# Optimization experiments

Measured on AMD Instinct MI355X. Metric: run time of the kernel, lower is better.

## Reference

```python
import jax, jax.numpy as jnp
import numpy as np

N_ITEMS = 50000; LM_IN = 768; D = 128; B = 256; L = 50
NH = 2; NL = 2; FF = 4 * D
TEMP = 0.1; BETA1 = 0.5; BETA2 = 0.5
NEG = -1e9


def _ln(x, g, b, eps=1e-5):
    m = x.mean(-1, keepdims=True)
    v = ((x - m) ** 2).mean(-1, keepdims=True)
    return (x - m) / jnp.sqrt(v + eps) * g + b


def _encoder(h, mask, P):
    # SASRec/BERT-style TransformerEncoder: pos-emb + LN, then NL blocks of
    # causal+padding-masked MHA and GELU FFN with post-LN residuals.
    pos, ln0g, ln0b, Wqkv, bqkv, Wo, bo, l1g, l1b, W1, b1, W2, b2, l2g, l2b = P
    Bh, Lh, Dh = h.shape
    dh = Dh // NH
    keep = jnp.tril(jnp.broadcast_to((mask != 0)[:, None, None, :], (Bh, 1, Lh, Lh)))
    bias = jnp.where(keep, 0.0, NEG)  # additive attention mask, [B,1,L,L]
    h = _ln(h + pos, ln0g, ln0b)
    scale = float(1.0 / np.sqrt(dh))
    for l in range(NL):
        qkv = h @ Wqkv[l] + bqkv[l]
        q, k, v = jnp.split(qkv, 3, axis=-1)
        sp = lambda t: t.reshape(Bh, Lh, NH, dh).transpose(0, 2, 1, 3)
        q, k, v = sp(q), sp(k), sp(v)
        att = jax.nn.softmax(jnp.einsum('bhqd,bhkd->bhqk', q, k) * scale + bias, axis=-1)
        o = jnp.einsum('bhqk,bhkd->bhqd', att, v).transpose(0, 2, 1, 3).reshape(Bh, Lh, Dh)
        h = _ln(h + o @ Wo[l] + bo[l], l1g[l], l1b[l])
        f = jax.nn.gelu(h @ W1[l] + b1[l]) @ W2[l] + b2[l]
        h = _ln(h + f, l2g[l], l2b[l])
    return h


def _last(trans, mask):
    # gather embedding at the last valid position: index = mask.sum(1) - 1
    idx = mask.sum(1).astype(jnp.int32) - 1
    return jnp.take_along_axis(trans, idx[:, None, None], axis=1)[:, 0]


def setup_inputs():
    key = jax.random.key(0)
    ks = jax.random.split(key, 32)
    s = 0.02

    def p(i, shape):
        return jax.random.normal(ks[i], shape, jnp.float32) * s

    inp = {}
    inp['x'] = jax.random.normal(ks[0], (N_ITEMS, LM_IN), jnp.float32)
    inp['uid'] = jax.random.randint(ks[1], (B,), 0, 100000)
    inp['edge_index'] = jax.random.randint(ks[2], (2, 1000), 0, N_ITEMS)
    inp['max_itemid'] = N_ITEMS - 1
    inp['itemid'] = jax.random.randint(ks[3], (B, L), 0, N_ITEMS)
    inp['mask'] = jnp.ones((B, L), jnp.float32)
    inp['id_emb'] = p(4, (N_ITEMS, D))
    inp['id_ln_g'] = jnp.ones(D); inp['id_ln_b'] = jnp.zeros(D)
    inp['text_W'] = p(5, (LM_IN, D)); inp['text_b'] = jnp.zeros(D)
    inp['text_ln_g'] = jnp.ones(D); inp['text_ln_b'] = jnp.zeros(D)
    for pre, base in (('ide_', 6), ('te_', 16)):
        inp[pre + 'pos'] = p(base, (L, D))
        inp[pre + 'ln0_g'] = jnp.ones(D); inp[pre + 'ln0_b'] = jnp.zeros(D)
        inp[pre + 'Wqkv'] = p(base + 1, (NL, D, 3 * D)); inp[pre + 'bqkv'] = jnp.zeros((NL, 3 * D))
        inp[pre + 'Wo'] = p(base + 2, (NL, D, D)); inp[pre + 'bo'] = jnp.zeros((NL, D))
        inp[pre + 'ln1_g'] = jnp.ones((NL, D)); inp[pre + 'ln1_b'] = jnp.zeros((NL, D))
        inp[pre + 'W1'] = p(base + 3, (NL, D, FF)); inp[pre + 'b1'] = jnp.zeros((NL, FF))
        inp[pre + 'W2'] = p(base + 4, (NL, FF, D)); inp[pre + 'b2'] = jnp.zeros((NL, D))
        inp[pre + 'ln2_g'] = jnp.ones((NL, D)); inp[pre + 'ln2_b'] = jnp.zeros((NL, D))
    return inp


def reference(x, uid, edge_index, max_itemid, itemid, mask,
              id_emb, id_ln_g, id_ln_b, text_W, text_b, text_ln_g, text_ln_b,
              ide_pos, ide_ln0_g, ide_ln0_b, ide_Wqkv, ide_bqkv, ide_Wo, ide_bo,
              ide_ln1_g, ide_ln1_b, ide_W1, ide_b1, ide_W2, ide_b2, ide_ln2_g, ide_ln2_b,
              te_pos, te_ln0_g, te_ln0_b, te_Wqkv, te_bqkv, te_Wo, te_bo,
              te_ln1_g, te_ln1_b, te_W1, te_b1, te_W2, te_b2, te_ln2_g, te_ln2_b):
    # --- ID module: layernorm over the full embedding table, gather, encode ---
    gnn_emb = _ln(id_emb, id_ln_g, id_ln_b)  # [n_items, D]
    ideP = (ide_pos, ide_ln0_g, ide_ln0_b, ide_Wqkv, ide_bqkv, ide_Wo, ide_bo,
            ide_ln1_g, ide_ln1_b, ide_W1, ide_b1, ide_W2, ide_b2, ide_ln2_g, ide_ln2_b)
    trans = _encoder(gnn_emb[itemid], mask, ideP)  # [B,L,D]
    session_emb = _last(trans, mask)  # [B,D]
    item_embs = gnn_emb[:max_itemid + 1]
    scores1 = session_emb @ item_embs.T  # [B, n_items]
    # --- Text module: linear+relu (dropout off at eval), layernorm, encode ---
    xmap = _ln(jax.nn.relu(x @ text_W + text_b), text_ln_g, text_ln_b)  # [n_items, D]
    teP = (te_pos, te_ln0_g, te_ln0_b, te_Wqkv, te_bqkv, te_Wo, te_bo,
           te_ln1_g, te_ln1_b, te_W1, te_b1, te_W2, te_b2, te_ln2_g, te_ln2_b)
    trans2 = _encoder(xmap[itemid], mask, teP)
    session_feat = _last(trans2, mask)
    scores2 = (session_feat @ xmap[:max_itemid + 1].T) / TEMP
    # eval path: combined score
    scores = BETA1 * scores1 + BETA2 * scores2
    return (scores, scores1, scores2, item_embs, gnn_emb[:max_itemid + 1], xmap[:max_itemid + 1])
```

## Files before the change

kernel.cpp:

```cpp
#include <hip/hip_runtime.h>

#define DEV __device__ __forceinline__

typedef float f32x4 __attribute__((ext_vector_type(4)));
typedef __bf16 bf16x8 __attribute__((ext_vector_type(8)));
#define MFMA16(a,b,c) __builtin_amdgcn_mfma_f32_16x16x32_bf16(a,b,c,0,0,0)

#define ASTRIDE 136
#define QSTRIDE 72
#define PSTRIDE 132

DEV float wsum(float v){
  #pragma unroll
  for (int o = 32; o > 0; o >>= 1) v += __shfl_xor(v, o, 64);
  return v;
}

DEV float gelu_f(float x){
  float u = 0.7978845608028654f * (x + 0.044715f * x * x * x);
  float e = __expf(2.f * u);
  float th = 1.f - 2.f / (e + 1.f);
  return 0.5f * x * (1.f + th);
}

__global__ __launch_bounds__(256) void ln_kernel(const float* in,
    float* out0, float* out1,
    const float* __restrict__ g, const float* __restrict__ bb, int nrows)
{
  int w = threadIdx.x >> 6, l = threadIdx.x & 63;
  int row = blockIdx.x * 4 + w;
  if (row >= nrows) return;
  const float* rp = in + (size_t)row * 128;
  float v0 = rp[l], v1 = rp[l + 64];
  float m = wsum(v0 + v1) * 0.0078125f;
  float d0 = v0 - m, d1 = v1 - m;
  float var = wsum(d0 * d0 + d1 * d1) * 0.0078125f;
  float rs = rsqrtf(var + 1e-5f);
  float o0 = d0 * rs * g[l] + bb[l];
  float o1 = d1 * rs * g[l + 64] + bb[l + 64];
  size_t base = (size_t)row * 128;
  out0[base + l] = o0; out0[base + l + 64] = o1;
  if (out1){ out1[base + l] = o0; out1[base + l + 64] = o1; }
}

__global__ __launch_bounds__(256) void prep_w(
    const float* __restrict__ Wa, const float* __restrict__ Wb,
    __bf16* __restrict__ dst, int K, int N, int nmat)
{
  int tid = blockIdx.x * 256 + threadIdx.x;
  int tpm = (N >> 4) * (K >> 5);
  if (tid >= nmat * tpm * 64) return;
  int lane = tid & 63;
  int tile = (tid >> 6) % tpm;
  int mat  = tid / (tpm * 64);
  const float* W;
  if (nmat == 1) W = Wa;
  else W = ((mat >> 1) ? Wb : Wa) + (size_t)(mat & 1) * K * N;
  int kdiv = K >> 5;
  int nt = tile / kdiv, kt = tile - nt * kdiv;
  int col  = nt * 16 + (lane & 15);
  int krow = kt * 32 + (lane >> 4) * 8;
  __bf16 v[8];
  #pragma unroll
  for (int j = 0; j < 8; j++) v[j] = (__bf16)W[(size_t)(krow + j) * N + col];
  *(bf16x8*)(dst + (size_t)tid * 8) = *(bf16x8*)v;
}

__global__ __launch_bounds__(256) void xmap_mfma(
    const float* __restrict__ X, const __bf16* __restrict__ wt,
    const float* __restrict__ bias, float* __restrict__ out)
{
  __shared__ __bf16 xb[64 * ASTRIDE];
  const int t = threadIdx.x, w = t >> 6, l = t & 63, lm = l & 15, quad = l >> 4;
  const int r0 = blockIdx.x * 64;
  f32x4 acc[8];
  #pragma unroll
  for (int nt = 0; nt < 8; nt++) acc[nt] = (f32x4){0.f,0.f,0.f,0.f};
  for (int kc = 0; kc < 6; kc++){
    for (int i = t; i < 64 * 32; i += 256){
      int r = i >> 5, c4 = (i & 31) * 4;
      float4 v = make_float4(0.f,0.f,0.f,0.f);
      if (r0 + r < 50000) v = *(const float4*)&X[(size_t)(r0 + r) * 768 + kc * 128 + c4];
      xb[r*ASTRIDE + c4 + 0] = (__bf16)v.x;
      xb[r*ASTRIDE + c4 + 1] = (__bf16)v.y;
      xb[r*ASTRIDE + c4 + 2] = (__bf16)v.z;
      xb[r*ASTRIDE + c4 + 3] = (__bf16)v.w;
    }
    __syncthreads();
    bf16x8 af[4];
    #pragma unroll
    for (int kt = 0; kt < 4; kt++)
      af[kt] = *(const bf16x8*)&xb[(w*16 + lm)*ASTRIDE + kt*32 + quad*8];
    #pragma unroll
    for (int nt = 0; nt < 8; nt++)
      #pragma unroll
      for (int kt = 0; kt < 4; kt++)
        acc[nt] = MFMA16(af[kt], *(const bf16x8*)(wt + ((size_t)(nt*24 + kc*4 + kt)*64 + l)*8), acc[nt]);
    __syncthreads();
  }
  #pragma unroll
  for (int nt = 0; nt < 8; nt++){
    int n = nt*16 + lm;
    float bs = bias[n];
    #pragma unroll
    for (int r = 0; r < 4; r++){
      int row = r0 + w*16 + quad*4 + r;
      if (row < 50000) out[(size_t)row*128 + n] = fmaxf(acc[nt][r] + bs, 0.f);
    }
  }
}

struct EncP {
  const float *pos, *ln0g, *ln0b, *bqkv, *bo, *ln1g, *ln1b, *b1, *b2, *ln2g, *ln2b;
  const __bf16 *wq, *wo, *w1, *w2;
  const float* emb;
  float* outT;
};

DEV void ln_reg(float res[8][4], const float* g, const float* bb, int lm){
  float gv[8], bv[8];
  #pragma unroll
  for (int nt = 0; nt < 8; nt++){ gv[nt] = g[nt*16 + lm]; bv[nt] = bb[nt*16 + lm]; }
  #pragma unroll
  for (int r = 0; r < 4; r++){
    float s = 0.f;
    #pragma unroll
    for (int nt = 0; nt < 8; nt++) s += res[nt][r];
    s += __shfl_xor(s, 1, 64); s += __shfl_xor(s, 2, 64);
    s += __shfl_xor(s, 4, 64); s += __shfl_xor(s, 8, 64);
    float mean = s * 0.0078125f;
    float v = 0.f;
    #pragma unroll
    for (int nt = 0; nt < 8; nt++){ float d = res[nt][r] - mean; v += d * d; }
    v += __shfl_xor(v, 1, 64); v += __shfl_xor(v, 2, 64);
    v += __shfl_xor(v, 4, 64); v += __shfl_xor(v, 8, 64);
    float rs = rsqrtf(v * 0.0078125f + 1e-5f);
    #pragma unroll
    for (int nt = 0; nt < 8; nt++)
      res[nt][r] = (res[nt][r] - mean) * rs * gv[nt] + bv[nt];
  }
}

DEV void stage_res(const float res[8][4], __bf16* ab, int mb, int quad, int lm){
  #pragma unroll
  for (int r = 0; r < 4; r++){
    int m = mb + quad*4 + r;
    #pragma unroll
    for (int nt = 0; nt < 8; nt++)
      ab[m*ASTRIDE + nt*16 + lm] = (__bf16)res[nt][r];
  }
}

__global__ __launch_bounds__(256, 4) void encoder_mfma(
    EncP P0, EncP P1, const int* __restrict__ itemid, const float* __restrict__ mask)
{
  EncP P = (blockIdx.x < 256) ? P0 : P1;
  const int b = blockIdx.x & 255;
  const int t = threadIdx.x, w = t >> 6, l = t & 63;
  const int lm = l & 15, quad = l >> 4;
  const int mb = w * 16;
  const int am = mb + lm;

  __shared__ __align__(16) char pool[35840];
  __bf16* ab = (__bf16*)pool;
  __bf16* kb = (__bf16*)(pool + 17408);
  __bf16* vb = (__bf16*)(pool + 17408 + 9216);
  float*  hfp = (float*)pool;
  __shared__ float maskv[64];

  if (t < 64) maskv[t] = (t < 50) ? mask[b*50 + t] : 0.f;

  for (int r = w; r < 50; r += 4){
    int it = itemid[b*50 + r];
    const float* er = P.emb + (size_t)it * 128;
    float v0 = er[l]      + P.pos[r*128 + l];
    float v1 = er[l + 64] + P.pos[r*128 + l + 64];
    float m = wsum(v0 + v1) * 0.0078125f;
    float d0 = v0 - m, d1 = v1 - m;
    float var = wsum(d0*d0 + d1*d1) * 0.0078125f;
    float rs = rsqrtf(var + 1e-5f);
    hfp[r*PSTRIDE + l]      = d0 * rs * P.ln0g[l] + P.ln0b[l];
    hfp[r*PSTRIDE + l + 64] = d1 * rs * P.ln0g[l + 64] + P.ln0b[l + 64];
  }
  __syncthreads();

  float res[8][4];
  #pragma unroll
  for (int r = 0; r < 4; r++){
    int m = mb + quad*4 + r;
    #pragma unroll
    for (int nt = 0; nt < 8; nt++)
      res[nt][r] = (m < 50) ? hfp[m*PSTRIDE + nt*16 + lm] : 0.f;
  }
  __syncthreads();

  for (int lay = 0; lay < 2; ++lay){
    const __bf16* wq = P.wq + lay * 49152;
    const __bf16* wo = P.wo + lay * 16384;
    const __bf16* w1 = P.w1 + lay * 65536;
    const __bf16* w2 = P.w2 + lay * 65536;
    const float* bq  = P.bqkv + lay * 384;
    const float* bo  = P.bo   + lay * 128;
    const float* g1  = P.ln1g + lay * 128;
    const float* b1n = P.ln1b + lay * 128;
    const float* b1f = P.b1   + lay * 512;
    const float* b2f = P.b2   + lay * 128;
    const float* g2  = P.ln2g + lay * 128;
    const float* b2n = P.ln2b + lay * 128;

    stage_res(res, ab, mb, quad, lm);
    bf16x8 afh[4];
    #pragma unroll
    for (int kt = 0; kt < 4; kt++)
      afh[kt] = *(const bf16x8*)&ab[am*ASTRIDE + kt*32 + quad*8];

    for (int hd = 0; hd < 2; hd++){
      __syncthreads();

      #pragma unroll
      for (int part = 0; part < 3; part++){
        #pragma unroll
        for (int tt = 0; tt < 4; tt++){
          int nt = part*8 + hd*4 + tt;
          f32x4 acc = (f32x4){0.f,0.f,0.f,0.f};
          #pragma unroll
          for (int kt = 0; kt < 4; kt++)
            acc = MFMA16(afh[kt], *(const bf16x8*)(wq + ((size_t)(nt*4 + kt)*64 + l)*8), acc);
          int n = nt*16 + lm;
          float bias = bq[n];
          int d = n & 63;
          #pragma unroll
          for (int r = 0; r < 4; r++){
            int m = mb + quad*4 + r;
            float v = acc[r] + bias;
            if (part == 0)      ab[m*ASTRIDE + 64 + d] = (__bf16)v;
            else if (part == 1) kb[m*QSTRIDE + d] = (__bf16)v;
            else                vb[d*QSTRIDE + m] = (__bf16)v;
          }
        }
      }
      __syncthreads();

      bf16x8 aq0 = *(const bf16x8*)&ab[am*ASTRIDE + 64 + quad*8];
      bf16x8 aq1 = *(const bf16x8*)&ab[am*ASTRIDE + 96 + quad*8];
      f32x4 sf[4];
      #pragma unroll
      for (int nt = 0; nt < 4; nt++){
        f32x4 acc = (f32x4){0.f,0.f,0.f,0.f};
        acc = MFMA16(aq0, *(const bf16x8*)&kb[(nt*16 + lm)*QSTRIDE + quad*8], acc);
        acc = MFMA16(aq1, *(const bf16x8*)&kb[(nt*16 + lm)*QSTRIDE + 32 + quad*8], acc);
        sf[nt] = acc;
      }
      #pragma unroll
      for (int r = 0; r < 4; r++){
        int q = mb + quad*4 + r;
        float sv[4];
        float mx = -3e38f;
        #pragma unroll
        for (int nt = 0; nt < 4; nt++){
          int ki = nt*16 + lm;
          float s = sf[nt][r] * 0.125f;
          bool keep = (ki <= q) && (maskv[ki] != 0.f);
          s = keep ? s : -1e9f;
          sv[nt] = s; mx = fmaxf(mx, s);
        }
        #pragma unroll
        for (int o = 1; o < 16; o <<= 1) mx = fmaxf(mx, __shfl_xor(mx, o, 64));
        float sum = 0.f;
        #pragma unroll
        for (int nt = 0; nt < 4; nt++){ float p = __expf(sv[nt] - mx); sv[nt] = p; sum += p; }
        #pragma unroll
        for (int o = 1; o < 16; o <<= 1) sum += __shfl_xor(sum, o, 64);
        float inv = 1.f / sum;
        #pragma unroll
        for (int nt = 0; nt < 4; nt++)
          ab[q*ASTRIDE + 64 + nt*16 + lm] = (__bf16)(sv[nt] * inv);
      }
      bf16x8 ap0 = *(const bf16x8*)&ab[am*ASTRIDE + 64 + quad*8];
      bf16x8 ap1 = *(const bf16x8*)&ab[am*ASTRIDE + 96 + quad*8];
      #pragma unroll
      for (int nt = 0; nt < 4; nt++){
        f32x4 acc = (f32x4){0.f,0.f,0.f,0.f};
        acc = MFMA16(ap0, *(const bf16x8*)&vb[(nt*16 + lm)*QSTRIDE + quad*8], acc);
        acc = MFMA16(ap1, *(const bf16x8*)&vb[(nt*16 + lm)*QSTRIDE + 32 + quad*8], acc);
        int dcol = hd*64 + nt*16 + lm;
        #pragma unroll
        for (int r = 0; r < 4; r++)
          ab[(mb + quad*4 + r)*ASTRIDE + dcol] = (__bf16)acc[r];
      }
    }

    {
      bf16x8 af[4];
      #pragma unroll
      for (int kt = 0; kt < 4; kt++)
        af[kt] = *(const bf16x8*)&ab[am*ASTRIDE + kt*32 + quad*8];
      #pragma unroll
      for (int nt = 0; nt < 8; nt++){
        f32x4 acc = (f32x4){0.f,0.f,0.f,0.f};
        #pragma unroll
        for (int kt = 0; kt < 4; kt++)
          acc = MFMA16(af[kt], *(const bf16x8*)(wo + ((size_t)(nt*4 + kt)*64 + l)*8), acc);
        float bias = bo[nt*16 + lm];
        #pragma unroll
        for (int r = 0; r < 4; r++)
          res[nt][r] += acc[r] + bias;
      }
    }
    ln_reg(res, g1, b1n, lm);

    stage_res(res, ab, mb, quad, lm);
    {
      bf16x8 ah[4];
      #pragma unroll
      for (int kt = 0; kt < 4; kt++)
        ah[kt] = *(const bf16x8*)&ab[am*ASTRIDE + kt*32 + quad*8];
      f32x4 acc2[8];
      #pragma unroll
      for (int nt = 0; nt < 8; nt++) acc2[nt] = (f32x4){0.f,0.f,0.f,0.f};
      for (int ch = 0; ch < 4; ch++){
        #pragma unroll
        for (int nt = 0; nt < 8; nt++){
          f32x4 acc = (f32x4){0.f,0.f,0.f,0.f};
          #pragma unroll
          for (int kt = 0; kt < 4; kt++)
            acc = MFMA16(ah[kt], *(const bf16x8*)(w1 + ((size_t)((ch*8 + nt)*4 + kt)*64 + l)*8), acc);
          float bias = b1f[ch*128 + nt*16 + lm];
          #pragma unroll
          for (int r = 0; r < 4; r++)
            ab[(mb + quad*4 + r)*ASTRIDE + nt*16 + lm] = (__bf16)gelu_f(acc[r] + bias);
        }
        bf16x8 a2[4];
        #pragma unroll
        for (int kt = 0; kt < 4; kt++)
          a2[kt] = *(const bf16x8*)&ab[am*ASTRIDE + kt*32 + quad*8];
        #pragma unroll
        for (int nt = 0; nt < 8; nt++)
          #pragma unroll
          for (int kt = 0; kt < 4; kt++)
            acc2[nt] = MFMA16(a2[kt], *(const bf16x8*)(w2 + ((size_t)(nt*16 + ch*4 + kt)*64 + l)*8), acc2[nt]);
      }
      #pragma unroll
      for (int nt = 0; nt < 8; nt++){
        float bias = b2f[nt*16 + lm];
        #pragma unroll
        for (int r = 0; r < 4; r++)
          res[nt][r] += acc2[nt][r] + bias;
      }
    }
    ln_reg(res, g2, b2n, lm);
  }

  {
    float sm = 0.f;
    for (int i = 0; i < 50; i++) sm += maskv[i];
    int idx = min(49, max(0, (int)sm - 1));
    #pragma unroll
    for (int r = 0; r < 4; r++){
      if (mb + quad*4 + r == idx){
        #pragma unroll
        for (int nt = 0; nt < 8; nt++)
          P.outT[(nt*16 + lm)*256 + b] = res[nt][r];
      }
    }
  }
}

__global__ __launch_bounds__(256) void scores_kernel(
    const float* __restrict__ seT, const float* __restrict__ sfT,
    const float* __restrict__ ie,  const float* __restrict__ xm,
    float* __restrict__ sc, float* __restrict__ s1, float* __restrict__ s2)
{
  __shared__ float iet[16 * 128];
  __shared__ float xmt[16 * 128];
  const int t = threadIdx.x;
  const size_t j0 = (size_t)blockIdx.x * 16;
  {
    const float4* ig = (const float4*)(ie + j0 * 128);
    const float4* xg = (const float4*)(xm + j0 * 128);
    float4* a = (float4*)iet; float4* c4 = (float4*)xmt;
    for (int i = t; i < 512; i += 256){ a[i] = ig[i]; c4[i] = xg[i]; }
  }
  __syncthreads();
  float a1[16], a2[16];
  #pragma unroll
  for (int j = 0; j < 16; j++){ a1[j] = 0.f; a2[j] = 0.f; }
  for (int k = 0; k < 128; k += 4){
    float se0 = seT[(k+0)*256 + t], se1 = seT[(k+1)*256 + t];
    float se2 = seT[(k+2)*256 + t], se3 = seT[(k+3)*256 + t];
    float sf0 = sfT[(k+0)*256 + t], sf1 = sfT[(k+1)*256 + t];
    float sf2 = sfT[(k+2)*256 + t], sf3 = sfT[(k+3)*256 + t];
    #pragma unroll
    for (int j = 0; j < 16; j++){
      float4 iv = *(const float4*)&iet[j*128 + k];
      float4 xv = *(const float4*)&xmt[j*128 + k];
      a1[j] += iv.x*se0 + iv.y*se1 + iv.z*se2 + iv.w*se3;
      a2[j] += xv.x*sf0 + xv.y*sf1 + xv.z*sf2 + xv.w*sf3;
    }
  }
  size_t rb = (size_t)t * 50000 + j0;
  #pragma unroll
  for (int j = 0; j < 16; j += 4){
    float4 v1 = make_float4(a1[j], a1[j+1], a1[j+2], a1[j+3]);
    float4 v2 = make_float4(a2[j]*10.f, a2[j+1]*10.f, a2[j+2]*10.f, a2[j+3]*10.f);
    float4 vs = make_float4(0.5f*(v1.x+v2.x), 0.5f*(v1.y+v2.y),
                            0.5f*(v1.z+v2.z), 0.5f*(v1.w+v2.w));
    *(float4*)&s1[rb + j] = v1;
    *(float4*)&s2[rb + j] = v2;
    *(float4*)&sc[rb + j] = vs;
  }
}

extern "C" void kernel_launch(void* const* d_in, const int* in_sizes, int n_in,
                              void* d_out, int out_size, void* d_ws, size_t ws_size,
                              hipStream_t stream)
{
  const float* x       = (const float*)d_in[0];
  const int*   itemid  = (const int*)d_in[4];
  const float* mask    = (const float*)d_in[5];
  const float* id_emb  = (const float*)d_in[6];
  const float* id_g    = (const float*)d_in[7];
  const float* id_b    = (const float*)d_in[8];
  const float* text_W  = (const float*)d_in[9];
  const float* text_b  = (const float*)d_in[10];
  const float* text_g  = (const float*)d_in[11];
  const float* text_bb = (const float*)d_in[12];

  float* out = (float*)d_out;
  float* o_scores = out;
  float* o_s1     = out + 12800000;
  float* o_s2     = out + 25600000;
  float* o_item   = out + 38400000;
  float* o_gnn    = out + 44800000;
  float* o_xmap   = out + 51200000;

  float* seT = (float*)d_ws;
  float* sfT = seT + 32768;
  __bf16* wp   = (__bf16*)((char*)d_ws + 262144);
  __bf16* wqkv = wp;
  __bf16* wo   = wp + 196608;
  __bf16* w1p  = wp + 262144;
  __bf16* w2p  = wp + 524288;
  __bf16* wtx  = wp + 786432;

  prep_w<<<96, 256, 0, stream>>>((const float*)d_in[16], (const float*)d_in[31], wqkv, 128, 384, 4);
  prep_w<<<32, 256, 0, stream>>>((const float*)d_in[18], (const float*)d_in[33], wo,   128, 128, 4);
  prep_w<<<128,256, 0, stream>>>((const float*)d_in[22], (const float*)d_in[37], w1p,  128, 512, 4);
  prep_w<<<128,256, 0, stream>>>((const float*)d_in[24], (const float*)d_in[39], w2p,  512, 128, 4);
  prep_w<<<48, 256, 0, stream>>>(text_W, text_W, wtx, 768, 128, 1);

  ln_kernel<<<12500, 256, 0, stream>>>(id_emb, o_item, o_gnn, id_g, id_b, 50000);
  xmap_mfma<<<782, 256, 0, stream>>>(x, wtx, text_b, o_xmap);
  ln_kernel<<<12500, 256, 0, stream>>>(o_xmap, o_xmap, nullptr, text_g, text_bb, 50000);

  EncP P0, P1;
  P0.pos = (const float*)d_in[13]; P0.ln0g = (const float*)d_in[14]; P0.ln0b = (const float*)d_in[15];
  P0.bqkv = (const float*)d_in[17]; P0.bo = (const float*)d_in[19];
  P0.ln1g = (const float*)d_in[20]; P0.ln1b = (const float*)d_in[21];
  P0.b1 = (const float*)d_in[23]; P0.b2 = (const float*)d_in[25];
  P0.ln2g = (const float*)d_in[26]; P0.ln2b = (const float*)d_in[27];
  P0.wq = wqkv; P0.wo = wo; P0.w1 = w1p; P0.w2 = w2p;
  P0.emb = o_item; P0.outT = seT;

  P1.pos = (const float*)d_in[28]; P1.ln0g = (const float*)d_in[29]; P1.ln0b = (const float*)d_in[30];
  P1.bqkv = (const float*)d_in[32]; P1.bo = (const float*)d_in[34];
  P1.ln1g = (const float*)d_in[35]; P1.ln1b = (const float*)d_in[36];
  P1.b1 = (const float*)d_in[38]; P1.b2 = (const float*)d_in[40];
  P1.ln2g = (const float*)d_in[41]; P1.ln2b = (const float*)d_in[42];
  P1.wq = wqkv + 2*49152; P1.wo = wo + 2*16384; P1.w1 = w1p + 2*65536; P1.w2 = w2p + 2*65536;
  P1.emb = o_xmap; P1.outT = sfT;

  encoder_mfma<<<512, 256, 0, stream>>>(P0, P1, itemid, mask);

  scores_kernel<<<3125, 256, 0, stream>>>(seT, sfT, o_item, o_xmap,
                                          o_scores, o_s1, o_s2);
}
```

Measured before the change: 904.8 us.

## Compute QKV for both heads at once with separate per-head LDS buffers

Runs the QKV projection for both heads in a single pass, writing Q, K and V into dedicated per-head shared-memory buffers. This removes one barrier per head and a redundant one after the initial load. Shared memory grows from about 35 KB to about 72 KB, and launch bounds drop to 2 blocks per CU, which lowers occupancy. The intent is fewer synchronisations and a longer run of back-to-back MFMA work.

```diff
diff --git a/kernel.cpp b/kernel.cpp
--- a/kernel.cpp
+++ b/kernel.cpp
@@ -151,7 +151,7 @@
   }
 }
 
-__global__ __launch_bounds__(256, 4) void encoder_mfma(
+__global__ __launch_bounds__(256, 2) void encoder_mfma(
     EncP P0, EncP P1, const int* __restrict__ itemid, const float* __restrict__ mask)
 {
   EncP P = (blockIdx.x < 256) ? P0 : P1;
@@ -161,11 +161,12 @@
   const int mb = w * 16;
   const int am = mb + lm;
 
-  __shared__ __align__(16) char pool[35840];
-  __bf16* ab = (__bf16*)pool;
-  __bf16* kb = (__bf16*)(pool + 17408);
-  __bf16* vb = (__bf16*)(pool + 17408 + 9216);
-  float*  hfp = (float*)pool;
+  __shared__ __align__(16) char pool[72704];
+  __bf16* ab   = (__bf16*)pool;
+  __bf16* qbuf = (__bf16*)(pool + 17408);
+  __bf16* kb   = (__bf16*)(pool + 35840);
+  __bf16* vb   = (__bf16*)(pool + 54272);
+  float*  hfp  = (float*)pool;
   __shared__ float maskv[64];
 
   if (t < 64) maskv[t] = (t < 50) ? mask[b*50 + t] : 0.f;
@@ -192,7 +193,6 @@
     for (int nt = 0; nt < 8; nt++)
       res[nt][r] = (m < 50) ? hfp[m*PSTRIDE + nt*16 + lm] : 0.f;
   }
-  __syncthreads();
 
   for (int lay = 0; lay < 2; ++lay){
     const __bf16* wq = P.wq + lay * 49152;
@@ -208,47 +208,50 @@
     const float* g2  = P.ln2g + lay * 128;
     const float* b2n = P.ln2b + lay * 128;
 
+    __syncthreads();
+
     stage_res(res, ab, mb, quad, lm);
     bf16x8 afh[4];
     #pragma unroll
     for (int kt = 0; kt < 4; kt++)
       afh[kt] = *(const bf16x8*)&ab[am*ASTRIDE + kt*32 + quad*8];
 
+    #pragma unroll
+    for (int nt = 0; nt < 24; nt++){
+      f32x4 acc = (f32x4){0.f,0.f,0.f,0.f};
+      #pragma unroll
+      for (int kt = 0; kt < 4; kt++)
+        acc = MFMA16(afh[kt], *(const bf16x8*)(wq + ((size_t)(nt*4 + kt)*64 + l)*8), acc);
+      int n = nt*16 + lm;
+      float bias = bq[n];
+      int part = n >> 7, hd = (n >> 6) & 1, d = n & 63;
+      __bf16* q_ = qbuf + hd*64*QSTRIDE;
+      __bf16* k_ = kb   + hd*64*QSTRIDE;
+      __bf16* v_ = vb   + hd*64*QSTRIDE;
+      #pragma unroll
+      for (int r = 0; r < 4; r++){
+        int m = mb + quad*4 + r;
+        float v = acc[r] + bias;
+        if (part == 0)      q_[m*QSTRIDE + d] = (__bf16)v;
+        else if (part == 1) k_[m*QSTRIDE + d] = (__bf16)v;
+        else                v_[d*QSTRIDE + m] = (__bf16)v;
+      }
+    }
+    __syncthreads();
+
+    #pragma unroll
     for (int hd = 0; hd < 2; hd++){
-      __syncthreads();
-
-      #pragma unroll
-      for (int part = 0; part < 3; part++){
-        #pragma unroll
-        for (int tt = 0; tt < 4; tt++){
-          int nt = part*8 + hd*4 + tt;
-          f32x4 acc = (f32x4){0.f,0.f,0.f,0.f};
-          #pragma unroll
-          for (int kt = 0; kt < 4; kt++)
-            acc = MFMA16(afh[kt], *(const bf16x8*)(wq + ((size_t)(nt*4 + kt)*64 + l)*8), acc);
-          int n = nt*16 + lm;
-          float bias = bq[n];
-          int d = n & 63;
-          #pragma unroll
-          for (int r = 0; r < 4; r++){
-            int m = mb + quad*4 + r;
-            float v = acc[r] + bias;
-            if (part == 0)      ab[m*ASTRIDE + 64 + d] = (__bf16)v;
-            else if (part == 1) kb[m*QSTRIDE + d] = (__bf16)v;
-            else                vb[d*QSTRIDE + m] = (__bf16)v;
-          }
-        }
-      }
-      __syncthreads();
-
-      bf16x8 aq0 = *(const bf16x8*)&ab[am*ASTRIDE + 64 + quad*8];
-      bf16x8 aq1 = *(const bf16x8*)&ab[am*ASTRIDE + 96 + quad*8];
+      __bf16* q_ = qbuf + hd*64*QSTRIDE;
+      const __bf16* k_ = kb + hd*64*QSTRIDE;
+      const __bf16* v_ = vb + hd*64*QSTRIDE;
+      bf16x8 aq0 = *(const bf16x8*)&q_[am*QSTRIDE + quad*8];
+      bf16x8 aq1 = *(const bf16x8*)&q_[am*QSTRIDE + 32 + quad*8];
       f32x4 sf[4];
       #pragma unroll
       for (int nt = 0; nt < 4; nt++){
         f32x4 acc = (f32x4){0.f,0.f,0.f,0.f};
-        acc = MFMA16(aq0, *(const bf16x8*)&kb[(nt*16 + lm)*QSTRIDE + quad*8], acc);
-        acc = MFMA16(aq1, *(const bf16x8*)&kb[(nt*16 + lm)*QSTRIDE + 32 + quad*8], acc);
+        acc = MFMA16(aq0, *(const bf16x8*)&k_[(nt*16 + lm)*QSTRIDE + quad*8], acc);
+        acc = MFMA16(aq1, *(const bf16x8*)&k_[(nt*16 + lm)*QSTRIDE + 32 + quad*8], acc);
         sf[nt] = acc;
       }
       #pragma unroll
@@ -274,15 +277,15 @@
         float inv = 1.f / sum;
         #pragma unroll
         for (int nt = 0; nt < 4; nt++)
-          ab[q*ASTRIDE + 64 + nt*16 + lm] = (__bf16)(sv[nt] * inv);
-      }
-      bf16x8 ap0 = *(const bf16x8*)&ab[am*ASTRIDE + 64 + quad*8];
-      bf16x8 ap1 = *(const bf16x8*)&ab[am*ASTRIDE + 96 + quad*8];
+          q_[q*QSTRIDE + nt*16 + lm] = (__bf16)(sv[nt] * inv);
+      }
+      bf16x8 ap0 = *(const bf16x8*)&q_[am*QSTRIDE + quad*8];
+      bf16x8 ap1 = *(const bf16x8*)&q_[am*QSTRIDE + 32 + quad*8];
       #pragma unroll
       for (int nt = 0; nt < 4; nt++){
         f32x4 acc = (f32x4){0.f,0.f,0.f,0.f};
-        acc = MFMA16(ap0, *(const bf16x8*)&vb[(nt*16 + lm)*QSTRIDE + quad*8], acc);
-        acc = MFMA16(ap1, *(const bf16x8*)&vb[(nt*16 + lm)*QSTRIDE + 32 + quad*8], acc);
+        acc = MFMA16(ap0, *(const bf16x8*)&v_[(nt*16 + lm)*QSTRIDE + quad*8], acc);
+        acc = MFMA16(ap1, *(const bf16x8*)&v_[(nt*16 + lm)*QSTRIDE + 32 + quad*8], acc);
         int dcol = hd*64 + nt*16 + lm;
         #pragma unroll
         for (int r = 0; r < 4; r++)
```

Measured after the change: 832.7 us. 1.09x faster.
